# Kernel optimization log

Measured on AMD Instinct MI355X. Metric: run time of the kernel, lower is better.

The kernel has to match this reference:

```python
import jax, jax.numpy as jnp
import numpy as np

ROUTING_ITERATIONS = 3


def squash(x):
    # squared norm over the capsule output dim
    sq = jnp.sum(x * x, axis=-1, keepdims=True)
    scale = sq / (1.0 + sq)
    return scale * x / jnp.sqrt(sq)


def setup_inputs() -> dict:
    key = jax.random.key(0)
    k1, k2 = jax.random.split(key)
    B, N, IN_C, K, OUT_C = 256, 1152, 8, 10, 16
    u = jax.random.normal(k1, (B, N, IN_C), dtype=jnp.float32)
    W = jax.random.normal(k2, (K, N, IN_C, OUT_C), dtype=jnp.float32)
    return {"u": u, "W": W}


def reference(u, W):
    # u: [B, N, in_c]; W: [K, N, in_c, out_c]
    # torch: u_hat = matmul(u[None,:,:,None,:], W[:,None]) -> [K, B, N, 1, out_c]
    u_hat = jnp.einsum('bni,knio->kbno', u, W)  # [K, B, N, out_c]
    b_ij = jnp.zeros_like(u_hat)
    v_j = None
    for it in range(ROUTING_ITERATIONS):
        c_ij = jax.nn.softmax(b_ij, axis=2)               # softmax over N, per out_c channel
        s_j = jnp.sum(c_ij * u_hat, axis=2, keepdims=True)  # [K, B, 1, out_c]
        v_j = squash(s_j)
        if it < ROUTING_ITERATIONS - 1:
            a_ij = jnp.sum(u_hat * v_j, axis=-1, keepdims=True)  # [K, B, N, 1]
            b_ij = b_ij + a_ij
    # match torch output shape [K, B, 1, 1, out_c]
    return v_j[:, :, :, None, :]
```

## Files before the change

### kernel.cpp

```cpp
#include <hip/hip_runtime.h>
#include <hip/hip_fp16.h>

#define Bsz 256
#define Nn  1152
#define Kk  10
#define NT  576
#define NW  9
#define SJ  1154

#define W_ELEMS (Kk*Nn*128)
#define U_ELEMS (Bsz*Nn*8)

__device__ __forceinline__ unsigned pkh2(float x, float y) {
    __half2 h = __floats2half2_rn(x, y);
    return *reinterpret_cast<unsigned*>(&h);
}
__device__ __forceinline__ float2 uph2(unsigned v) {
    __half2 h;
    *reinterpret_cast<unsigned*>(&h) = v;
    return __half22float2(h);
}
__device__ __forceinline__ void up8(const uint4 q, float f[8]) {
    float2 a = uph2(q.x), b = uph2(q.y), c = uph2(q.z), d = uph2(q.w);
    f[0]=a.x; f[1]=a.y; f[2]=b.x; f[3]=b.y; f[4]=c.x; f[5]=c.y; f[6]=d.x; f[7]=d.y;
}

__global__ void cvt_kernel(const float* __restrict__ W, const float* __restrict__ u,
                           __half2* __restrict__ Wh, __half2* __restrict__ uh) {
    const int idx = blockIdx.x * blockDim.x + threadIdx.x;
    const int wg = W_ELEMS / 8;
    const float4* p;
    __half2* o;
    if (idx < wg) {
        p = (const float4*)W + (size_t)idx * 2;
        o = Wh + (size_t)idx * 4;
    } else {
        const int j = idx - wg;
        p = (const float4*)u + (size_t)j * 2;
        o = uh + (size_t)j * 4;
    }
    const float4 a = p[0], b = p[1];
    o[0] = __floats2half2_rn(a.x, a.y);
    o[1] = __floats2half2_rn(a.z, a.w);
    o[2] = __floats2half2_rn(b.x, b.y);
    o[3] = __floats2half2_rn(b.z, b.w);
}

template<bool HALF>
__global__ __launch_bounds__(NT, 2)
void digitcaps_kernel(const float* __restrict__ u32, const float* __restrict__ W32,
                      const __half* __restrict__ uh, const __half* __restrict__ Wh,
                      float* __restrict__ out)
{
    const int t    = threadIdx.x;
    const int lane = t & 63;
    const int wav  = t >> 6;
    const int bg   = blockIdx.x;
    const int k    = blockIdx.y;
    const int b0   = bg * 2;

    __shared__ uint2    uhS[8 * SJ];
    __shared__ unsigned cS2[Nn];
    __shared__ float    redS[2 * NW * 17];
    __shared__ __align__(16) float vS[32];
    __shared__ float    mS[2];

    {
        const int oh   = t & 1;
        const int nsub = t >> 1;
        for (int r = 0; r < 4; ++r) {
            const int n = r * 288 + nsub;
            float ua[8], ub[8];
            if (HALF) {
                const uint4 qa = *(const uint4*)(uh + ((size_t)b0 * Nn + n) * 8);
                const uint4 qb = *(const uint4*)(uh + ((size_t)(b0 + 1) * Nn + n) * 8);
                up8(qa, ua); up8(qb, ub);
            } else {
                const float4* up0 = (const float4*)(u32 + ((size_t)b0 * Nn + n) * 8);
                const float4* up1 = (const float4*)(u32 + ((size_t)(b0 + 1) * Nn + n) * 8);
                const float4 x0 = up0[0], x1 = up0[1];
                const float4 y0 = up1[0], y1 = up1[1];
                ua[0]=x0.x; ua[1]=x0.y; ua[2]=x0.z; ua[3]=x0.w;
                ua[4]=x1.x; ua[5]=x1.y; ua[6]=x1.z; ua[7]=x1.w;
                ub[0]=y0.x; ub[1]=y0.y; ub[2]=y0.z; ub[3]=y0.w;
                ub[4]=y1.x; ub[5]=y1.y; ub[6]=y1.z; ub[7]=y1.w;
            }
            float a0[8], a1[8];
            #pragma unroll
            for (int o = 0; o < 8; ++o) { a0[o] = 0.f; a1[o] = 0.f; }
            #pragma unroll
            for (int i = 0; i < 8; ++i) {
                float wv[8];
                if (HALF) {
                    const uint4 qw = *(const uint4*)(Wh + ((size_t)(k * Nn + n)) * 128 + i * 16 + oh * 8);
                    up8(qw, wv);
                } else {
                    const float4* wp = (const float4*)(W32 + ((size_t)k * Nn + n) * 128) + oh * 2 + i * 4;
                    const float4 w0 = wp[0], w1 = wp[1];
                    wv[0]=w0.x; wv[1]=w0.y; wv[2]=w0.z; wv[3]=w0.w;
                    wv[4]=w1.x; wv[5]=w1.y; wv[6]=w1.z; wv[7]=w1.w;
                }
                const float x = ua[i], y = ub[i];
                #pragma unroll
                for (int o = 0; o < 8; ++o) { a0[o] += x * wv[o]; a1[o] += y * wv[o]; }
            }
            #pragma unroll
            for (int jj = 0; jj < 4; ++jj) {
                const int j = oh * 4 + jj;
                uhS[j * SJ + n] = make_uint2(pkh2(a0[2*jj], a0[2*jj+1]),
                                             pkh2(a1[2*jj], a1[2*jj+1]));
            }
        }
    }
    __syncthreads();

    float lg0[2] = {0.f, 0.f}, lg1[2] = {0.f, 0.f};
    float v0[16], v1[16];
    const int j_s = lane & 7;
    const int g_s = lane >> 3;

    for (int it = 0; it < 3; ++it) {
        if (it > 0) {
            #pragma unroll
            for (int r = 0; r < 2; ++r) {
                const int n = t + r * NT;
                float acc0 = 0.f, acc1 = 0.f;
                #pragma unroll
                for (int j = 0; j < 8; ++j) {
                    const uint2 q = uhS[j * SJ + n];
                    const float2 f0 = uph2(q.x);
                    const float2 f1 = uph2(q.y);
                    acc0 += f0.x * v0[2*j] + f0.y * v0[2*j+1];
                    acc1 += f1.x * v1[2*j] + f1.y * v1[2*j+1];
                }
                lg0[r] += acc0;
                lg1[r] += acc1;
            }
            float m0 = fmaxf(lg0[0], lg0[1]);
            float m1 = fmaxf(lg1[0], lg1[1]);
            #pragma unroll
            for (int off = 1; off <= 32; off <<= 1) {
                m0 = fmaxf(m0, __shfl_xor(m0, off));
                m1 = fmaxf(m1, __shfl_xor(m1, off));
            }
            if (lane == 0) { redS[wav] = m0; redS[NW + wav] = m1; }
            __syncthreads();
            if (t < 2) {
                float m = redS[t * NW];
                for (int w = 1; w < NW; ++w) m = fmaxf(m, redS[t * NW + w]);
                mS[t] = m;
            }
            __syncthreads();
            m0 = mS[0]; m1 = mS[1];
            const float e00 = __expf(lg0[0] - m0), e01 = __expf(lg0[1] - m0);
            const float e10 = __expf(lg1[0] - m1), e11 = __expf(lg1[1] - m1);
            cS2[t]      = pkh2(e00, e10);
            cS2[t + NT] = pkh2(e01, e11);
            __syncthreads();
        }

        float2 sp0 = {0.f, 0.f}, sp1 = {0.f, 0.f};
        float dp0 = 0.f, dp1 = 0.f;
        #pragma unroll
        for (int cc = 0; cc < 16; ++cc) {
            const int n = cc * 72 + wav * 8 + g_s;
            float c0, c1;
            if (it == 0) { c0 = 1.f; c1 = 1.f; }
            else { const float2 c2 = uph2(cS2[n]); c0 = c2.x; c1 = c2.y; }
            const uint2 q = uhS[j_s * SJ + n];
            const float2 f0 = uph2(q.x);
            const float2 f1 = uph2(q.y);
            sp0.x += c0 * f0.x; sp0.y += c0 * f0.y;
            sp1.x += c1 * f1.x; sp1.y += c1 * f1.y;
            dp0 += c0; dp1 += c1;
        }
        #pragma unroll
        for (int off = 8; off <= 32; off <<= 1) {
            sp0.x += __shfl_xor(sp0.x, off);
            sp0.y += __shfl_xor(sp0.y, off);
            sp1.x += __shfl_xor(sp1.x, off);
            sp1.y += __shfl_xor(sp1.y, off);
            dp0   += __shfl_xor(dp0,   off);
            dp1   += __shfl_xor(dp1,   off);
        }
        if (lane < 8) {
            redS[(0*NW + wav)*17 + 2*j_s    ] = sp0.x;
            redS[(0*NW + wav)*17 + 2*j_s + 1] = sp0.y;
            redS[(1*NW + wav)*17 + 2*j_s    ] = sp1.x;
            redS[(1*NW + wav)*17 + 2*j_s + 1] = sp1.y;
        }
        if (lane == 0) {
            redS[(0*NW + wav)*17 + 16] = dp0;
            redS[(1*NW + wav)*17 + 16] = dp1;
        }
        __syncthreads();

        if (t < 32) {
            const int b = t >> 4, o = t & 15;
            float s = 0.f, d = 0.f;
            #pragma unroll
            for (int w = 0; w < NW; ++w) {
                s += redS[(b*NW + w)*17 + o];
                d += redS[(b*NW + w)*17 + 16];
            }
            s /= d;
            float s2 = s * s;
            #pragma unroll
            for (int off = 1; off <= 8; off <<= 1) s2 += __shfl_xor(s2, off);
            const float scale = (s2 / (1.f + s2)) * rsqrtf(fmaxf(s2, 1e-30f));
            const float v = s * scale;
            vS[b*16 + o] = v;
            if (it == 2) out[((size_t)k * Bsz + b0 + b) * 16 + o] = v;
        }
        if (it == 2) break;
        __syncthreads();

        {
            const float4* vp = (const float4*)vS;
            #pragma unroll
            for (int q4 = 0; q4 < 4; ++q4) {
                *(float4*)&v0[4*q4] = vp[q4];
                *(float4*)&v1[4*q4] = vp[4 + q4];
            }
        }
    }
}

extern "C" void kernel_launch(void* const* d_in, const int* in_sizes, int n_in,
                              void* d_out, int out_size, void* d_ws, size_t ws_size,
                              hipStream_t stream) {
    const float* u = (const float*)d_in[0];
    const float* W = (const float*)d_in[1];
    float* out = (float*)d_out;
    const size_t need = (size_t)(W_ELEMS + U_ELEMS) * sizeof(__half);
    if (ws_size >= need) {
        __half* Wh = (__half*)d_ws;
        __half* uh = (__half*)((char*)d_ws + (size_t)W_ELEMS * sizeof(__half));
        cvt_kernel<<<dim3((W_ELEMS + U_ELEMS) / 8 / 256), dim3(256), 0, stream>>>(
            W, u, (__half2*)Wh, (__half2*)uh);
        digitcaps_kernel<true><<<dim3(128, 10), dim3(NT), 0, stream>>>(
            nullptr, nullptr, uh, Wh, out);
    } else {
        digitcaps_kernel<false><<<dim3(128, 10), dim3(NT), 0, stream>>>(
            u, W, nullptr, nullptr, out);
    }
}
```

Measured before the change: 130.4 us.

## Process one batch element per block and fuse first routing sum into projection

Each block now handles a single batch element with 384 threads instead of two elements with 576 threads, doubling the grid and raising the occupancy target. The u_hat tile in shared memory becomes n-major with 16-byte rows, and the first iteration's weighted sum is accumulated during the projection pass, skipping a separate LDS sweep. The cost is that each W slice is now loaded twice as often from global/L2 memory.

Result: slower. 141.5 us (+8.5%).

```diff
diff --git a/kernel.cpp b/kernel.cpp
--- a/kernel.cpp
+++ b/kernel.cpp
@@ -4,9 +4,8 @@
 #define Bsz 256
 #define Nn  1152
 #define Kk  10
-#define NT  576
-#define NW  9
-#define SJ  1154
+#define NT  384
+#define NW  6
 
 #define W_ELEMS (Kk*Nn*128)
 #define U_ELEMS (Bsz*Nn*8)
@@ -47,7 +46,7 @@
 }
 
 template<bool HALF>
-__global__ __launch_bounds__(NT, 2)
+__global__ __launch_bounds__(NT, 6)
 void digitcaps_kernel(const float* __restrict__ u32, const float* __restrict__ W32,
                       const __half* __restrict__ uh, const __half* __restrict__ Wh,
                       float* __restrict__ out)
@@ -55,153 +54,136 @@
     const int t    = threadIdx.x;
     const int lane = t & 63;
     const int wav  = t >> 6;
-    const int bg   = blockIdx.x;
+    const int b    = blockIdx.x;
     const int k    = blockIdx.y;
-    const int b0   = bg * 2;
-
-    __shared__ uint2    uhS[8 * SJ];
-    __shared__ unsigned cS2[Nn];
-    __shared__ float    redS[2 * NW * 17];
-    __shared__ __align__(16) float vS[32];
-    __shared__ float    mS[2];
+
+    __shared__ unsigned uhS[Nn * 8];
+    __shared__ __half   cS[Nn];
+    __shared__ float    redS[NW * 17];
+    __shared__ __align__(16) float vS[16];
+    __shared__ float    mS;
 
     {
         const int oh   = t & 1;
         const int nsub = t >> 1;
-        for (int r = 0; r < 4; ++r) {
-            const int n = r * 288 + nsub;
-            float ua[8], ub[8];
+        float sacc[8];
+        #pragma unroll
+        for (int o = 0; o < 8; ++o) sacc[o] = 0.f;
+        for (int r = 0; r < 6; ++r) {
+            const int n = r * 192 + nsub;
+            float ua[8];
             if (HALF) {
-                const uint4 qa = *(const uint4*)(uh + ((size_t)b0 * Nn + n) * 8);
-                const uint4 qb = *(const uint4*)(uh + ((size_t)(b0 + 1) * Nn + n) * 8);
-                up8(qa, ua); up8(qb, ub);
+                up8(*(const uint4*)(uh + ((size_t)b * Nn + n) * 8), ua);
             } else {
-                const float4* up0 = (const float4*)(u32 + ((size_t)b0 * Nn + n) * 8);
-                const float4* up1 = (const float4*)(u32 + ((size_t)(b0 + 1) * Nn + n) * 8);
-                const float4 x0 = up0[0], x1 = up0[1];
-                const float4 y0 = up1[0], y1 = up1[1];
+                const float4* up = (const float4*)(u32 + ((size_t)b * Nn + n) * 8);
+                const float4 x0 = up[0], x1 = up[1];
                 ua[0]=x0.x; ua[1]=x0.y; ua[2]=x0.z; ua[3]=x0.w;
                 ua[4]=x1.x; ua[5]=x1.y; ua[6]=x1.z; ua[7]=x1.w;
-                ub[0]=y0.x; ub[1]=y0.y; ub[2]=y0.z; ub[3]=y0.w;
-                ub[4]=y1.x; ub[5]=y1.y; ub[6]=y1.z; ub[7]=y1.w;
-            }
-            float a0[8], a1[8];
-            #pragma unroll
-            for (int o = 0; o < 8; ++o) { a0[o] = 0.f; a1[o] = 0.f; }
+            }
+            float a0[8];
+            #pragma unroll
+            for (int o = 0; o < 8; ++o) a0[o] = 0.f;
             #pragma unroll
             for (int i = 0; i < 8; ++i) {
                 float wv[8];
                 if (HALF) {
-                    const uint4 qw = *(const uint4*)(Wh + ((size_t)(k * Nn + n)) * 128 + i * 16 + oh * 8);
-                    up8(qw, wv);
+                    up8(*(const uint4*)(Wh + ((size_t)(k * Nn + n)) * 128 + i * 16 + oh * 8), wv);
                 } else {
-                    const float4* wp = (const float4*)(W32 + ((size_t)k * Nn + n) * 128) + oh * 2 + i * 4;
+                    const float4* wp = (const float4*)(W32 + ((size_t)k * Nn + n) * 128 + i * 16 + oh * 8);
                     const float4 w0 = wp[0], w1 = wp[1];
                     wv[0]=w0.x; wv[1]=w0.y; wv[2]=w0.z; wv[3]=w0.w;
                     wv[4]=w1.x; wv[5]=w1.y; wv[6]=w1.z; wv[7]=w1.w;
                 }
-                const float x = ua[i], y = ub[i];
+                const float x = ua[i];
                 #pragma unroll
-                for (int o = 0; o < 8; ++o) { a0[o] += x * wv[o]; a1[o] += y * wv[o]; }
-            }
-            #pragma unroll
-            for (int jj = 0; jj < 4; ++jj) {
-                const int j = oh * 4 + jj;
-                uhS[j * SJ + n] = make_uint2(pkh2(a0[2*jj], a0[2*jj+1]),
-                                             pkh2(a1[2*jj], a1[2*jj+1]));
-            }
+                for (int o = 0; o < 8; ++o) a0[o] += x * wv[o];
+            }
+            *(uint4*)&uhS[n * 8 + oh * 4] =
+                make_uint4(pkh2(a0[0], a0[1]), pkh2(a0[2], a0[3]),
+                           pkh2(a0[4], a0[5]), pkh2(a0[6], a0[7]));
+            #pragma unroll
+            for (int o = 0; o < 8; ++o) sacc[o] += a0[o];
+        }
+        #pragma unroll
+        for (int off = 2; off <= 32; off <<= 1)
+            #pragma unroll
+            for (int o = 0; o < 8; ++o) sacc[o] += __shfl_xor(sacc[o], off);
+        if (lane < 2) {
+            #pragma unroll
+            for (int o = 0; o < 8; ++o) redS[wav * 17 + lane * 8 + o] = sacc[o];
         }
     }
     __syncthreads();
 
-    float lg0[2] = {0.f, 0.f}, lg1[2] = {0.f, 0.f};
-    float v0[16], v1[16];
+    float lg[3] = {0.f, 0.f, 0.f};
+    float v0[16];
     const int j_s = lane & 7;
     const int g_s = lane >> 3;
 
     for (int it = 0; it < 3; ++it) {
         if (it > 0) {
-            #pragma unroll
-            for (int r = 0; r < 2; ++r) {
+            const float4* vp = (const float4*)vS;
+            #pragma unroll
+            for (int q4 = 0; q4 < 4; ++q4) *(float4*)&v0[4*q4] = vp[q4];
+            #pragma unroll
+            for (int r = 0; r < 3; ++r) {
                 const int n = t + r * NT;
-                float acc0 = 0.f, acc1 = 0.f;
+                float fa[8], fb[8];
+                up8(*(const uint4*)&uhS[n * 8], fa);
+                up8(*(const uint4*)&uhS[n * 8 + 4], fb);
+                float acc = 0.f;
                 #pragma unroll
-                for (int j = 0; j < 8; ++j) {
-                    const uint2 q = uhS[j * SJ + n];
-                    const float2 f0 = uph2(q.x);
-                    const float2 f1 = uph2(q.y);
-                    acc0 += f0.x * v0[2*j] + f0.y * v0[2*j+1];
-                    acc1 += f1.x * v1[2*j] + f1.y * v1[2*j+1];
-                }
-                lg0[r] += acc0;
-                lg1[r] += acc1;
-            }
-            float m0 = fmaxf(lg0[0], lg0[1]);
-            float m1 = fmaxf(lg1[0], lg1[1]);
-            #pragma unroll
-            for (int off = 1; off <= 32; off <<= 1) {
-                m0 = fmaxf(m0, __shfl_xor(m0, off));
-                m1 = fmaxf(m1, __shfl_xor(m1, off));
-            }
-            if (lane == 0) { redS[wav] = m0; redS[NW + wav] = m1; }
-            __syncthreads();
-            if (t < 2) {
-                float m = redS[t * NW];
-                for (int w = 1; w < NW; ++w) m = fmaxf(m, redS[t * NW + w]);
-                mS[t] = m;
-            }
-            __syncthreads();
-            m0 = mS[0]; m1 = mS[1];
-            const float e00 = __expf(lg0[0] - m0), e01 = __expf(lg0[1] - m0);
-            const float e10 = __expf(lg1[0] - m1), e11 = __expf(lg1[1] - m1);
-            cS2[t]      = pkh2(e00, e10);
-            cS2[t + NT] = pkh2(e01, e11);
-            __syncthreads();
-        }
-
-        float2 sp0 = {0.f, 0.f}, sp1 = {0.f, 0.f};
-        float dp0 = 0.f, dp1 = 0.f;
-        #pragma unroll
-        for (int cc = 0; cc < 16; ++cc) {
-            const int n = cc * 72 + wav * 8 + g_s;
-            float c0, c1;
-            if (it == 0) { c0 = 1.f; c1 = 1.f; }
-            else { const float2 c2 = uph2(cS2[n]); c0 = c2.x; c1 = c2.y; }
-            const uint2 q = uhS[j_s * SJ + n];
-            const float2 f0 = uph2(q.x);
-            const float2 f1 = uph2(q.y);
-            sp0.x += c0 * f0.x; sp0.y += c0 * f0.y;
-            sp1.x += c1 * f1.x; sp1.y += c1 * f1.y;
-            dp0 += c0; dp1 += c1;
-        }
-        #pragma unroll
-        for (int off = 8; off <= 32; off <<= 1) {
-            sp0.x += __shfl_xor(sp0.x, off);
-            sp0.y += __shfl_xor(sp0.y, off);
-            sp1.x += __shfl_xor(sp1.x, off);
-            sp1.y += __shfl_xor(sp1.y, off);
-            dp0   += __shfl_xor(dp0,   off);
-            dp1   += __shfl_xor(dp1,   off);
-        }
-        if (lane < 8) {
-            redS[(0*NW + wav)*17 + 2*j_s    ] = sp0.x;
-            redS[(0*NW + wav)*17 + 2*j_s + 1] = sp0.y;
-            redS[(1*NW + wav)*17 + 2*j_s    ] = sp1.x;
-            redS[(1*NW + wav)*17 + 2*j_s + 1] = sp1.y;
-        }
-        if (lane == 0) {
-            redS[(0*NW + wav)*17 + 16] = dp0;
-            redS[(1*NW + wav)*17 + 16] = dp1;
-        }
-        __syncthreads();
-
-        if (t < 32) {
-            const int b = t >> 4, o = t & 15;
-            float s = 0.f, d = 0.f;
-            #pragma unroll
-            for (int w = 0; w < NW; ++w) {
-                s += redS[(b*NW + w)*17 + o];
-                d += redS[(b*NW + w)*17 + 16];
+                for (int o = 0; o < 8; ++o) acc += fa[o] * v0[o] + fb[o] * v0[8 + o];
+                lg[r] += acc;
+            }
+            float m = fmaxf(fmaxf(lg[0], lg[1]), lg[2]);
+            #pragma unroll
+            for (int off = 1; off <= 32; off <<= 1) m = fmaxf(m, __shfl_xor(m, off));
+            if (lane == 0) redS[wav] = m;
+            __syncthreads();
+            if (t == 0) {
+                float mm = redS[0];
+                for (int w = 1; w < NW; ++w) mm = fmaxf(mm, redS[w]);
+                mS = mm;
+            }
+            __syncthreads();
+            m = mS;
+            cS[t]          = __float2half(__expf(lg[0] - m));
+            cS[t + NT]     = __float2half(__expf(lg[1] - m));
+            cS[t + 2*NT]   = __float2half(__expf(lg[2] - m));
+            __syncthreads();
+            float spx = 0.f, spy = 0.f, dp = 0.f;
+            #pragma unroll
+            for (int cc = 0; cc < 24; ++cc) {
+                const int n = cc * 48 + wav * 8 + g_s;
+                const float c = __half2float(cS[n]);
+                const float2 f = uph2(uhS[n * 8 + j_s]);
+                spx += c * f.x; spy += c * f.y; dp += c;
+            }
+            #pragma unroll
+            for (int off = 8; off <= 32; off <<= 1) {
+                spx += __shfl_xor(spx, off);
+                spy += __shfl_xor(spy, off);
+                dp  += __shfl_xor(dp,  off);
+            }
+            if (lane < 8) {
+                redS[wav * 17 + 2*j_s    ] = spx;
+                redS[wav * 17 + 2*j_s + 1] = spy;
+            }
+            if (lane == 0) redS[wav * 17 + 16] = dp;
+            __syncthreads();
+        }
+
+        if (t < 16) {
+            float s = 0.f;
+            #pragma unroll
+            for (int w = 0; w < NW; ++w) s += redS[w * 17 + t];
+            float d;
+            if (it == 0) d = (float)Nn;
+            else {
+                d = 0.f;
+                #pragma unroll
+                for (int w = 0; w < NW; ++w) d += redS[w * 17 + 16];
             }
             s /= d;
             float s2 = s * s;
@@ -209,20 +191,10 @@
             for (int off = 1; off <= 8; off <<= 1) s2 += __shfl_xor(s2, off);
             const float scale = (s2 / (1.f + s2)) * rsqrtf(fmaxf(s2, 1e-30f));
             const float v = s * scale;
-            vS[b*16 + o] = v;
-            if (it == 2) out[((size_t)k * Bsz + b0 + b) * 16 + o] = v;
-        }
-        if (it == 2) break;
+            vS[t] = v;
+            if (it == 2) out[((size_t)k * Bsz + b) * 16 + t] = v;
+        }
         __syncthreads();
-
-        {
-            const float4* vp = (const float4*)vS;
-            #pragma unroll
-            for (int q4 = 0; q4 < 4; ++q4) {
-                *(float4*)&v0[4*q4] = vp[q4];
-                *(float4*)&v1[4*q4] = vp[4 + q4];
-            }
-        }
     }
 }
 
@@ -235,13 +207,13 @@
     const size_t need = (size_t)(W_ELEMS + U_ELEMS) * sizeof(__half);
     if (ws_size >= need) {
         __half* Wh = (__half*)d_ws;
-        __half* uh = (__half*)((char*)d_ws + (size_t)W_ELEMS * sizeof(__half));
+        __half* uhp = (__half*)((char*)d_ws + (size_t)W_ELEMS * sizeof(__half));
         cvt_kernel<<<dim3((W_ELEMS + U_ELEMS) / 8 / 256), dim3(256), 0, stream>>>(
-            W, u, (__half2*)Wh, (__half2*)uh);
-        digitcaps_kernel<true><<<dim3(128, 10), dim3(NT), 0, stream>>>(
-            nullptr, nullptr, uh, Wh, out);
+            W, u, (__half2*)Wh, (__half2*)uhp);
+        digitcaps_kernel<true><<<dim3(Bsz, Kk), dim3(NT), 0, stream>>>(
+            nullptr, nullptr, uhp, Wh, out);
     } else {
-        digitcaps_kernel<false><<<dim3(128, 10), dim3(NT), 0, stream>>>(
+        digitcaps_kernel<false><<<dim3(Bsz, Kk), dim3(NT), 0, stream>>>(
             u, W, nullptr, nullptr, out);
     }
 }
```
